# Kernel optimization log

Hardware: AMD Instinct MI355X
Metric: run time of the kernel (lower is better)

## Reference

```python
import jax, jax.numpy as jnp
import numpy as np

S, L, T, E, H = 88, 10, 30, 768, 64  # stocks, lookback days, texts/day, embed, hidden


def setup_inputs() -> dict:
    ks = iter(jax.random.split(jax.random.key(0), 40))

    def p(shape, s=0.05):
        return (jax.random.normal(next(ks), shape) * s).astype(jnp.float32)

    inp = {
        'text_inputs': jax.random.normal(next(ks), (S, L, T, E), jnp.float32),
        'time_inputs': jax.random.uniform(next(ks), (S, L, T), jnp.float32),
        # per-stock TimeLSTM params (torch Linear stored as [in,out])
        'Wd_w': p((S, H, H)), 'Wd_b': p((S, H)),
        'Wall_w': p((S, H, 4 * H)), 'Wall_b': p((S, 4 * H)),
        'Uall_w': p((S, E, 4 * H)), 'Uall_b': p((S, 4 * H)),
        # per-stock text attention
        'tW1_w': p((S, H, H)), 'tW1_b': p((S, H)),
        'tW2_w': p((S, H, H)), 'tW2_b': p((S, H)),
        'tV_w': p((S, H, 1)), 'tV_b': p((S, 1)),
        # per-stock day nn.LSTM cell (h0=0 so W_hh contributes nothing; keep its bias)
        'ih_w': p((S, H, 4 * H)), 'ih_b': p((S, 4 * H)), 'hh_b': p((S, 4 * H)),
        # per-stock day attention
        'dW1_w': p((S, H, H)), 'dW1_b': p((S, H)),
        'dW2_w': p((S, H, H)), 'dW2_b': p((S, H)),
        'dV_w': p((S, H, 1)), 'dV_b': p((S, 1)),
        # shared prediction head
        'pred_w': p((H, 1)), 'pred_b': p((1,)),
    }
    return inp


def _fast_forward(text_inputs, time_inputs, Wd_w, Wd_b, Wall_w, Wall_b, Uall_w, Uall_b,
                  tW1_w, tW1_b, tW2_w, tW2_b, tV_w, tV_b,
                  ih_w, ih_b, hh_b, dW1_w, dW1_b, dW2_w, dW2_b, dV_w, dV_b,
                  pred_w, pred_b):
    # Precompute input projection U_all(x): [S,L,T,4H]
    u = jnp.einsum('slte,seg->sltg', text_inputs, Uall_w) + Uall_b[:, None, None, :]

    def step(carry, xs):
        h, c = carry                      # each [S,L,H]
        u_t, ts_t = xs                    # [S,L,4H], [S,L]
        c_s1 = jnp.tanh(jnp.einsum('slh,shk->slk', c, Wd_w) + Wd_b[:, None, :])
        c_adj = c - c_s1 + c_s1 * ts_t[..., None]
        gates = jnp.einsum('slh,shg->slg', h, Wall_w) + Wall_b[:, None, :] + u_t
        f, i, o, g = jnp.split(jax.nn.sigmoid(gates), 4, axis=-1)  # all sigmoid (incl. candidate, as in source)
        c = f * c_adj + i * g
        h = o * jnp.tanh(c)
        return (h, c), h

    z = jnp.zeros((S, L, H), text_inputs.dtype)
    (h_last, _), hs = jax.lax.scan(step, (z, z), (jnp.moveaxis(u, 2, 0), jnp.moveaxis(time_inputs, 2, 0)))
    full = jnp.moveaxis(hs, 0, 2)  # [S,L,T,H]

    # text attention: softmax over texts T
    a1 = jnp.einsum('slh,shk->slk', h_last, tW1_w) + tW1_b[:, None, :]
    a2 = jnp.einsum('slth,shk->sltk', full, tW2_w) + tW2_b[:, None, None, :]
    score = jnp.einsum('slth,sho->slto', jnp.tanh(a1[:, :, None, :] + a2), tV_w) + tV_b[:, None, None, :]
    attn = jax.nn.softmax(score, axis=2)
    day_vec = jnp.sum(attn * full, axis=2)  # [S,L,H]

    # day nn.LSTM: input (1,L,64) seq-first => seq_len=1, batch=L -> single step from zero state
    gates = jnp.einsum('slh,shg->slg', day_vec, ih_w) + ih_b[:, None, :] + hh_b[:, None, :]
    i_g, f_g, g_g, o_g = jnp.split(gates, 4, axis=-1)  # torch gate order i,f,g,o
    c_d = jax.nn.sigmoid(i_g) * jnp.tanh(g_g)
    h_d = jax.nn.sigmoid(o_g) * jnp.tanh(c_d)  # [S,L,H]; output == h_n since seq_len==1

    # day attention: full == last == h_d, softmax over days L
    b1 = jnp.einsum('slh,shk->slk', h_d, dW1_w) + dW1_b[:, None, :]
    b2 = jnp.einsum('slh,shk->slk', h_d, dW2_w) + dW2_b[:, None, :]
    score_d = jnp.einsum('slh,sho->slo', jnp.tanh(b1 + b2), dV_w) + dV_b[:, None, :]
    attn_d = jax.nn.softmax(score_d, axis=1)
    stock_vec = jnp.sum(attn_d * h_d, axis=1)  # [S,H]

    return jax.nn.leaky_relu(stock_vec @ pred_w + pred_b)  # [S,1], slope 0.01


def reference(text_inputs, time_inputs, Wd_w, Wd_b, Wall_w, Wall_b, Uall_w, Uall_b,
              tW1_w, tW1_b, tW2_w, tW2_b, tV_w, tV_b,
              ih_w, ih_b, hh_b, dW1_w, dW1_b, dW2_w, dW2_b, dV_w, dV_b,
              pred_w, pred_b):
    return _fast_forward(text_inputs, time_inputs, Wd_w, Wd_b, Wall_w, Wall_b, Uall_w, Uall_b,
                         tW1_w, tW1_b, tW2_w, tW2_b, tV_w, tV_b,
                         ih_w, ih_b, hh_b, dW1_w, dW1_b, dW2_w, dW2_b, dV_w, dV_b,
                         pred_w, pred_b)
```

## Files before the change

kernel.cpp:

```cpp
#include <hip/hip_runtime.h>
#include <cmath>

#define NS 88
#define NL 10
#define NT 30
#define NE 768
#define NH 64
#define NG 256
#define NM 300

typedef _Float16 half_t;
typedef __attribute__((ext_vector_type(2))) _Float16 half2_t;
typedef __attribute__((ext_vector_type(8))) _Float16 half8;
typedef __attribute__((ext_vector_type(4))) _Float16 half4v;
typedef __attribute__((ext_vector_type(4))) float f32x4;

__device__ inline void gload_lds16(const void* g, void* l) {
  __builtin_amdgcn_global_load_lds(
      (const __attribute__((address_space(1))) unsigned int*)g,
      (__attribute__((address_space(3))) unsigned int*)l, 16, 0, 0);
}

__device__ inline float fsigmoid(float x) {
  return __builtin_amdgcn_rcpf(1.f + __expf(-x));
}
__device__ inline float ftanh(float x) {
  float e = __expf(2.f * x);
  return 1.f - 2.f * __builtin_amdgcn_rcpf(e + 1.f);
}

#if __has_builtin(__builtin_amdgcn_fdot2)
__device__ inline float fdot2(half2_t a, half2_t b, float c) {
  return __builtin_amdgcn_fdot2(a, b, c, false);
}
#else
__device__ inline float fdot2(half2_t a, half2_t b, float c) {
  return fmaf((float)a[1], (float)b[1], fmaf((float)a[0], (float)b[0], c));
}
#endif

__device__ inline half2_t mk_h2(float a, float b) {
  half2_t r; r[0] = (half_t)a; r[1] = (half_t)b; return r;
}

__global__ __launch_bounds__(256) void convB_kernel(
    const float* __restrict__ in, half_t* __restrict__ out)
{
  __shared__ float tile[32][36];
  int b  = blockIdx.x;
  int s  = b / 192;
  int r  = b % 192;
  int kt = r / 8;
  int nt = r % 8;
  int t  = threadIdx.x;

  int kk  = t >> 3;
  int nn4 = (t & 7) * 4;
  float4 v = *(const float4*)(in + ((size_t)s * NE + kt * 32 + kk) * NG + nt * 32 + nn4);
  tile[kk][nn4 + 0] = v.x; tile[kk][nn4 + 1] = v.y;
  tile[kk][nn4 + 2] = v.z; tile[kk][nn4 + 3] = v.w;
  __syncthreads();

  int nn = t >> 3;
  int kq = (t & 7) * 4;
  half4v o;
#pragma unroll
  for (int j = 0; j < 4; ++j) o[j] = (half_t)tile[kq + j][nn];
  *(half4v*)(out + ((size_t)s * NG + nt * 32 + nn) * NE + kt * 32 + kq) = o;
}

__global__ __launch_bounds__(256) void gemm_mfma_kernel(
    const float*  __restrict__ text,
    const half_t* __restrict__ Bf16,
    const float*  __restrict__ bias,
    float* __restrict__ U)
{
  __shared__ uint4 smem4[1536];
  char* smem = (char*)smem4;

  int b   = blockIdx.x;
  int swz = (b & 7) * 110 + (b >> 3);
  int s   = swz / 10;
  int rr_ = swz % 10;
  int m0  = (rr_ >> 1) * 64;
  int n0  = (rr_ & 1) * 128;

  int tid = threadIdx.x;
  int w = tid >> 6, l = tid & 63;
  int wm = w >> 1, wn = w & 1;
  int lr = l & 15, lk = l >> 4;

  const float*  At = text + (size_t)s * NM * NE;
  const half_t* Bb = Bf16 + ((size_t)s * NG + n0) * NE;

  f32x4 acc[2][4];
#pragma unroll
  for (int i = 0; i < 2; ++i)
#pragma unroll
    for (int j = 0; j < 4; ++j) acc[i][j] = (f32x4){0.f, 0.f, 0.f, 0.f};

  for (int step = 0; step < 12; ++step) {
    int k0 = step * 64;
#pragma unroll
    for (int j = 0; j < 4; ++j) {
      int ci  = j * 256 + tid;
      int row = ci >> 3;
      int c   = (ci & 7) ^ (row & 7);
      gload_lds16(Bb + (size_t)row * NE + k0 + c * 8,
                  smem + 8192 + j * 4096 + w * 1024);
    }
#pragma unroll
    for (int j = 0; j < 2; ++j) {
      int idx = j * 256 + tid;
      int row = idx >> 3, c = idx & 7;
      int m   = m0 + row;
      half8 av;
      if (m < NM) {
        const float* p = At + (size_t)m * NE + k0 + c * 8;
        float4 x = *(const float4*)p;
        float4 y = *(const float4*)(p + 4);
        av[0] = (half_t)x.x; av[1] = (half_t)x.y;
        av[2] = (half_t)x.z; av[3] = (half_t)x.w;
        av[4] = (half_t)y.x; av[5] = (half_t)y.y;
        av[6] = (half_t)y.z; av[7] = (half_t)y.w;
      } else {
#pragma unroll
        for (int q = 0; q < 8; ++q) av[q] = (half_t)0.f;
      }
      *(half8*)(smem + row * 128 + ((c ^ (row & 7)) * 16)) = av;
    }
    __syncthreads();

#pragma unroll
    for (int kk = 0; kk < 2; ++kk) {
      half8 af[2], bf[4];
#pragma unroll
      for (int fm = 0; fm < 2; ++fm) {
        int rw = wm * 32 + fm * 16 + lr;
        int cc = (kk * 4 + lk) ^ (rw & 7);
        af[fm] = *(const half8*)(smem + rw * 128 + cc * 16);
      }
#pragma unroll
      for (int fn = 0; fn < 4; ++fn) {
        int rw = wn * 64 + fn * 16 + lr;
        int cc = (kk * 4 + lk) ^ (rw & 7);
        bf[fn] = *(const half8*)(smem + 8192 + rw * 128 + cc * 16);
      }
#pragma unroll
      for (int fm = 0; fm < 2; ++fm)
#pragma unroll
        for (int fn = 0; fn < 4; ++fn)
          acc[fm][fn] = __builtin_amdgcn_mfma_f32_16x16x32_f16(
              af[fm], bf[fn], acc[fm][fn], 0, 0, 0);
    }
    __syncthreads();
  }

#pragma unroll
  for (int fn = 0; fn < 4; ++fn) {
    int col = n0 + wn * 64 + fn * 16 + lr;
    float bv = bias[(size_t)s * NG + col];
#pragma unroll
    for (int fm = 0; fm < 2; ++fm) {
      int mbase = m0 + wm * 32 + fm * 16 + lk * 4;
#pragma unroll
      for (int e = 0; e < 4; ++e) {
        int m = mbase + e;
        if (m < NM)
          U[((size_t)s * NM + m) * NG + col] = acc[fm][fn][e] + bv;
      }
    }
  }
}

__global__ __launch_bounds__(64) void lstm_attn_kernel(
    const float* __restrict__ u,
    const float* __restrict__ time_in,
    const float* __restrict__ Wdw,  const float* __restrict__ Wdb,
    const float* __restrict__ Wallw, const float* __restrict__ Wallb,
    const float* __restrict__ tW1w, const float* __restrict__ tW1b,
    const float* __restrict__ tW2w, const float* __restrict__ tW2b,
    const float* __restrict__ tVw,  const float* __restrict__ tVb,
    float* __restrict__ day_vec)
{
  int bid = blockIdx.x;
  int s = bid / NL;
  int j = threadIdx.x;

  __shared__ float   u_s[NT * NG];
  __shared__ float   hist[NT][NH];
  __shared__ float   ts_s[NT];
  __shared__ half2_t h2_s[NH / 2];
  __shared__ half2_t c2_s[NH / 2];

  const float* u_base = u + (size_t)bid * NT * NG;
#pragma unroll
  for (int i = 0; i < NT; ++i)
    gload_lds16(u_base + i * NG + j * 4, (char*)u_s + i * 1024);

  if (j < NT) ts_s[j] = time_in[(size_t)bid * NT + j];
  ((half_t*)h2_s)[j] = (half_t)0.f;
  ((half_t*)c2_s)[j] = (half_t)0.f;

  const float* Wa  = Wallw + (size_t)s * NH * NG;
  const float* Wdp = Wdw   + (size_t)s * NH * NH;
  half2_t wf[32], wi[32], wo[32], wg[32], wd[32];
#pragma unroll
  for (int k2 = 0; k2 < 32; ++k2) {
    wf[k2] = mk_h2(Wa[(2*k2) * NG + j],        Wa[(2*k2+1) * NG + j]);
    wi[k2] = mk_h2(Wa[(2*k2) * NG + 64 + j],   Wa[(2*k2+1) * NG + 64 + j]);
    wo[k2] = mk_h2(Wa[(2*k2) * NG + 128 + j],  Wa[(2*k2+1) * NG + 128 + j]);
    wg[k2] = mk_h2(Wa[(2*k2) * NG + 192 + j],  Wa[(2*k2+1) * NG + 192 + j]);
    wd[k2] = mk_h2(Wdp[(2*k2) * NH + j],       Wdp[(2*k2+1) * NH + j]);
  }
  float bf = Wallb[(size_t)s * NG + j];
  float bi = Wallb[(size_t)s * NG + 64 + j];
  float bo = Wallb[(size_t)s * NG + 128 + j];
  float bg = Wallb[(size_t)s * NG + 192 + j];
  float bd = Wdb[(size_t)s * NH + j];

  asm volatile("s_waitcnt vmcnt(0)" ::: "memory");

  float c_my = 0.f;
  for (int t = 0; t < NT; ++t) {
    float accf = bf + u_s[t * NG + j];
    float acci = bi + u_s[t * NG + 64 + j];
    float acco = bo + u_s[t * NG + 128 + j];
    float accg = bg + u_s[t * NG + 192 + j];
    float accd = bd;
#pragma unroll
    for (int k2 = 0; k2 < 32; ++k2) {
      half2_t hv = h2_s[k2];
      half2_t cv = c2_s[k2];
      accf = fdot2(hv, wf[k2], accf);
      acci = fdot2(hv, wi[k2], acci);
      acco = fdot2(hv, wo[k2], acco);
      accg = fdot2(hv, wg[k2], accg);
      accd = fdot2(cv, wd[k2], accd);
    }
    float f  = fsigmoid(accf);
    float ii = fsigmoid(acci);
    float o  = fsigmoid(acco);
    float gg = fsigmoid(accg);
    float cadj = c_my + ftanh(accd) * (ts_s[t] - 1.f);
    float cn = fmaf(f, cadj, ii * gg);
    c_my = cn;
    float hn = o * ftanh(cn);
    ((half_t*)h2_s)[j] = (half_t)hn;
    ((half_t*)c2_s)[j] = (half_t)cn;
    hist[t][j] = hn;
  }

  const float* tW1p = tW1w + (size_t)s * NH * NH;
  const float* tW2p = tW2w + (size_t)s * NH * NH;

  float tw2c[NH];
#pragma unroll
  for (int h = 0; h < NH; ++h) tw2c[h] = tW2p[(size_t)h * NH + j];

  float a1 = tW1b[(size_t)s * NH + j];
  {
    const float4* h4 = (const float4*)&hist[NT - 1][0];
#pragma unroll
    for (int q = 0; q < NH / 4; ++q) {
      float4 v = h4[q];
      a1 = fmaf(v.x, tW1p[(size_t)(4*q+0) * NH + j], a1);
      a1 = fmaf(v.y, tW1p[(size_t)(4*q+1) * NH + j], a1);
      a1 = fmaf(v.z, tW1p[(size_t)(4*q+2) * NH + j], a1);
      a1 = fmaf(v.w, tW1p[(size_t)(4*q+3) * NH + j], a1);
    }
  }
  float b2k = tW2b[(size_t)s * NH + j];
  float tv  = tVw[(size_t)s * NH + j];
  float tvb = tVb[s];

  float sc[NT];
#pragma unroll
  for (int t = 0; t < NT; ++t) {
    float a2 = b2k;
    const float4* h4 = (const float4*)&hist[t][0];
#pragma unroll
    for (int q = 0; q < NH / 4; ++q) {
      float4 v = h4[q];
      a2 = fmaf(v.x, tw2c[4*q+0], a2);
      a2 = fmaf(v.y, tw2c[4*q+1], a2);
      a2 = fmaf(v.z, tw2c[4*q+2], a2);
      a2 = fmaf(v.w, tw2c[4*q+3], a2);
    }
    float v = ftanh(a1 + a2) * tv;
#pragma unroll
    for (int off = 32; off >= 1; off >>= 1) v += __shfl_xor(v, off);
    sc[t] = v + tvb;
  }
  float mx = sc[0];
#pragma unroll
  for (int t = 1; t < NT; ++t) mx = fmaxf(mx, sc[t]);
  float sum = 0.f;
#pragma unroll
  for (int t = 0; t < NT; ++t) { sc[t] = __expf(sc[t] - mx); sum += sc[t]; }
  float inv = __builtin_amdgcn_rcpf(sum);
  float dv = 0.f;
#pragma unroll
  for (int t = 0; t < NT; ++t) dv = fmaf(sc[t] * inv, hist[t][j], dv);
  day_vec[(size_t)bid * NH + j] = dv;
}

__global__ __launch_bounds__(256) void day_head_kernel(
    const float* __restrict__ day_vec,
    const float* __restrict__ ihw, const float* __restrict__ ihb,
    const float* __restrict__ hhb,
    const float* __restrict__ dW1w, const float* __restrict__ dW1b,
    const float* __restrict__ dW2w, const float* __restrict__ dW2b,
    const float* __restrict__ dVw,  const float* __restrict__ dVb,
    const float* __restrict__ predw, const float* __restrict__ predb,
    float* __restrict__ out)
{
  int s = blockIdx.x;
  int g = threadIdx.x;
  int j = g & 63;
  int q = g >> 6;

  __shared__ float dv_s[NL][NH];
  __shared__ float gl[NL][NG];
  __shared__ float hd[NL][NH];

  for (int i = g; i < NL * NH; i += 256)
    ((float*)dv_s)[i] = day_vec[(size_t)s * NL * NH + i];
  __syncthreads();

  float ihcol[NH];
#pragma unroll
  for (int k = 0; k < NH; ++k)
    ihcol[k] = ihw[((size_t)s * NH + k) * NG + g];
  float bias = ihb[(size_t)s * NG + g] + hhb[(size_t)s * NG + g];

  bool is_gpart = (g >= 128 && g < 192);
  for (int l = 0; l < NL; ++l) {
    float acc = bias;
#pragma unroll
    for (int k = 0; k < NH; ++k) acc = fmaf(dv_s[l][k], ihcol[k], acc);
    gl[l][g] = is_gpart ? ftanh(acc) : fsigmoid(acc);
  }
  __syncthreads();
  for (int l = q; l < NL; l += 4) {
    float cd = gl[l][j] * gl[l][128 + j];
    hd[l][j] = gl[l][192 + j] * ftanh(cd);
  }
  __syncthreads();

  if (g < 64) {
    int k = g;
    float dw1c[NH], dw2c[NH];
#pragma unroll
    for (int h = 0; h < NH; ++h) {
      dw1c[h] = dW1w[((size_t)s * NH + h) * NH + k];
      dw2c[h] = dW2w[((size_t)s * NH + h) * NH + k];
    }
    float b1 = dW1b[(size_t)s * NH + k];
    float b2 = dW2b[(size_t)s * NH + k];
    float dv = dVw[(size_t)s * NH + k];
    float dvb = dVb[s];

    float sc[NL];
#pragma unroll
    for (int l = 0; l < NL; ++l) {
      float x1 = b1, x2 = b2;
#pragma unroll
      for (int h = 0; h < NH; ++h) {
        x1 = fmaf(hd[l][h], dw1c[h], x1);
        x2 = fmaf(hd[l][h], dw2c[h], x2);
      }
      float v = ftanh(x1 + x2) * dv;
#pragma unroll
      for (int off = 32; off >= 1; off >>= 1) v += __shfl_xor(v, off);
      sc[l] = v + dvb;
    }
    float mx = sc[0];
#pragma unroll
    for (int l = 1; l < NL; ++l) mx = fmaxf(mx, sc[l]);
    float sum = 0.f;
#pragma unroll
    for (int l = 0; l < NL; ++l) { sc[l] = __expf(sc[l] - mx); sum += sc[l]; }
    float inv = __builtin_amdgcn_rcpf(sum);
    float sv = 0.f;
#pragma unroll
    for (int l = 0; l < NL; ++l) sv = fmaf(sc[l] * inv, hd[l][k], sv);

    float p = sv * predw[k];
#pragma unroll
    for (int off = 32; off >= 1; off >>= 1) p += __shfl_xor(p, off);
    if (k == 0) {
      float x = p + predb[0];
      out[s] = (x >= 0.f) ? x : 0.01f * x;
    }
  }
}

extern "C" void kernel_launch(void* const* d_in, const int* in_sizes, int n_in,
                              void* d_out, int out_size, void* d_ws, size_t ws_size,
                              hipStream_t stream) {
  (void)in_sizes; (void)n_in; (void)out_size; (void)ws_size;

  const float* text    = (const float*)d_in[0];
  const float* time_in = (const float*)d_in[1];
  const float* Wdw     = (const float*)d_in[2];
  const float* Wdb     = (const float*)d_in[3];
  const float* Wallw   = (const float*)d_in[4];
  const float* Wallb   = (const float*)d_in[5];
  const float* Uallw   = (const float*)d_in[6];
  const float* Uallb   = (const float*)d_in[7];
  const float* tW1w    = (const float*)d_in[8];
  const float* tW1b    = (const float*)d_in[9];
  const float* tW2w    = (const float*)d_in[10];
  const float* tW2b    = (const float*)d_in[11];
  const float* tVw     = (const float*)d_in[12];
  const float* tVb     = (const float*)d_in[13];
  const float* ihw     = (const float*)d_in[14];
  const float* ihb     = (const float*)d_in[15];
  const float* hhb     = (const float*)d_in[16];
  const float* dW1w    = (const float*)d_in[17];
  const float* dW1b    = (const float*)d_in[18];
  const float* dW2w    = (const float*)d_in[19];
  const float* dW2b    = (const float*)d_in[20];
  const float* dVw     = (const float*)d_in[21];
  const float* dVb     = (const float*)d_in[22];
  const float* predw   = (const float*)d_in[23];
  const float* predb   = (const float*)d_in[24];

  float* ws      = (float*)d_ws;
  float* u       = ws;
  float* day_vec = u + (size_t)NS * NM * NG;
  half_t* Bf16   = (half_t*)(day_vec + (size_t)NS * NL * NH);

  convB_kernel<<<NS * 192, 256, 0, stream>>>(Uallw, Bf16);
  gemm_mfma_kernel<<<NS * 10, 256, 0, stream>>>(text, Bf16, Uallb, u);
  lstm_attn_kernel<<<NS * NL, 64, 0, stream>>>(u, time_in, Wdw, Wdb,
                                               Wallw, Wallb,
                                               tW1w, tW1b, tW2w, tW2b,
                                               tVw, tVb, day_vec);
  day_head_kernel<<<NS, 256, 0, stream>>>(day_vec, ihw, ihb, hhb,
                                          dW1w, dW1b, dW2w, dW2b, dVw, dVb,
                                          predw, predb, (float*)d_out);
}
```

Before: 104.7 us.

## Fuse U-projection GEMM into per-(stock,day) LSTM kernel, keeping U in LDS

Merges the MFMA GEMM producing the input projection into the TimeLSTM kernel. Each block computes the 30x256 projection for one (stock, day) directly into shared memory, then one wave runs the recurrence. This removes the global write and re-read of the large U tensor and one kernel launch. In exchange, each block reloads the full per-stock fp16 weight matrix, raising L2 traffic tenfold, pads 30 rows to 32, and idles three waves during the recurrence.

Result: slower. 136.3 us (+30.1%).

```diff
diff --git a/kernel.cpp b/kernel.cpp
--- a/kernel.cpp
+++ b/kernel.cpp
@@ -69,112 +69,10 @@
   *(half4v*)(out + ((size_t)s * NG + nt * 32 + nn) * NE + kt * 32 + kq) = o;
 }
 
-__global__ __launch_bounds__(256) void gemm_mfma_kernel(
+__global__ __launch_bounds__(256, 2) void fused_kernel(
     const float*  __restrict__ text,
     const half_t* __restrict__ Bf16,
-    const float*  __restrict__ bias,
-    float* __restrict__ U)
-{
-  __shared__ uint4 smem4[1536];
-  char* smem = (char*)smem4;
-
-  int b   = blockIdx.x;
-  int swz = (b & 7) * 110 + (b >> 3);
-  int s   = swz / 10;
-  int rr_ = swz % 10;
-  int m0  = (rr_ >> 1) * 64;
-  int n0  = (rr_ & 1) * 128;
-
-  int tid = threadIdx.x;
-  int w = tid >> 6, l = tid & 63;
-  int wm = w >> 1, wn = w & 1;
-  int lr = l & 15, lk = l >> 4;
-
-  const float*  At = text + (size_t)s * NM * NE;
-  const half_t* Bb = Bf16 + ((size_t)s * NG + n0) * NE;
-
-  f32x4 acc[2][4];
-#pragma unroll
-  for (int i = 0; i < 2; ++i)
-#pragma unroll
-    for (int j = 0; j < 4; ++j) acc[i][j] = (f32x4){0.f, 0.f, 0.f, 0.f};
-
-  for (int step = 0; step < 12; ++step) {
-    int k0 = step * 64;
-#pragma unroll
-    for (int j = 0; j < 4; ++j) {
-      int ci  = j * 256 + tid;
-      int row = ci >> 3;
-      int c   = (ci & 7) ^ (row & 7);
-      gload_lds16(Bb + (size_t)row * NE + k0 + c * 8,
-                  smem + 8192 + j * 4096 + w * 1024);
-    }
-#pragma unroll
-    for (int j = 0; j < 2; ++j) {
-      int idx = j * 256 + tid;
-      int row = idx >> 3, c = idx & 7;
-      int m   = m0 + row;
-      half8 av;
-      if (m < NM) {
-        const float* p = At + (size_t)m * NE + k0 + c * 8;
-        float4 x = *(const float4*)p;
-        float4 y = *(const float4*)(p + 4);
-        av[0] = (half_t)x.x; av[1] = (half_t)x.y;
-        av[2] = (half_t)x.z; av[3] = (half_t)x.w;
-        av[4] = (half_t)y.x; av[5] = (half_t)y.y;
-        av[6] = (half_t)y.z; av[7] = (half_t)y.w;
-      } else {
-#pragma unroll
-        for (int q = 0; q < 8; ++q) av[q] = (half_t)0.f;
-      }
-      *(half8*)(smem + row * 128 + ((c ^ (row & 7)) * 16)) = av;
-    }
-    __syncthreads();
-
-#pragma unroll
-    for (int kk = 0; kk < 2; ++kk) {
-      half8 af[2], bf[4];
-#pragma unroll
-      for (int fm = 0; fm < 2; ++fm) {
-        int rw = wm * 32 + fm * 16 + lr;
-        int cc = (kk * 4 + lk) ^ (rw & 7);
-        af[fm] = *(const half8*)(smem + rw * 128 + cc * 16);
-      }
-#pragma unroll
-      for (int fn = 0; fn < 4; ++fn) {
-        int rw = wn * 64 + fn * 16 + lr;
-        int cc = (kk * 4 + lk) ^ (rw & 7);
-        bf[fn] = *(const half8*)(smem + 8192 + rw * 128 + cc * 16);
-      }
-#pragma unroll
-      for (int fm = 0; fm < 2; ++fm)
-#pragma unroll
-        for (int fn = 0; fn < 4; ++fn)
-          acc[fm][fn] = __builtin_amdgcn_mfma_f32_16x16x32_f16(
-              af[fm], bf[fn], acc[fm][fn], 0, 0, 0);
-    }
-    __syncthreads();
-  }
-
-#pragma unroll
-  for (int fn = 0; fn < 4; ++fn) {
-    int col = n0 + wn * 64 + fn * 16 + lr;
-    float bv = bias[(size_t)s * NG + col];
-#pragma unroll
-    for (int fm = 0; fm < 2; ++fm) {
-      int mbase = m0 + wm * 32 + fm * 16 + lk * 4;
-#pragma unroll
-      for (int e = 0; e < 4; ++e) {
-        int m = mbase + e;
-        if (m < NM)
-          U[((size_t)s * NM + m) * NG + col] = acc[fm][fn][e] + bv;
-      }
-    }
-  }
-}
-
-__global__ __launch_bounds__(64) void lstm_attn_kernel(
-    const float* __restrict__ u,
+    const float*  __restrict__ ubias,
     const float* __restrict__ time_in,
     const float* __restrict__ Wdw,  const float* __restrict__ Wdb,
     const float* __restrict__ Wallw, const float* __restrict__ Wallb,
@@ -183,22 +81,108 @@
     const float* __restrict__ tVw,  const float* __restrict__ tVb,
     float* __restrict__ day_vec)
 {
-  int bid = blockIdx.x;
-  int s = bid / NL;
-  int j = threadIdx.x;
-
-  __shared__ float   u_s[NT * NG];
+  __shared__ float   u_s[32 * NG];
+  __shared__ uint4   Bbuf4[2048];
+  __shared__ uint4   Abuf4[256];
   __shared__ float   hist[NT][NH];
   __shared__ float   ts_s[NT];
   __shared__ half2_t h2_s[NH / 2];
   __shared__ half2_t c2_s[NH / 2];
-
-  const float* u_base = u + (size_t)bid * NT * NG;
-#pragma unroll
-  for (int i = 0; i < NT; ++i)
-    gload_lds16(u_base + i * NG + j * 4, (char*)u_s + i * 1024);
-
-  if (j < NT) ts_s[j] = time_in[(size_t)bid * NT + j];
+  char* Bbuf = (char*)Bbuf4;
+  char* Abuf = (char*)Abuf4;
+
+  int b   = blockIdx.x;
+  int bid = (b & 7) * 110 + (b >> 3);
+  int s   = bid / NL;
+  int tid = threadIdx.x;
+  int w = tid >> 6, l = tid & 63;
+  int lr = l & 15, lk = l >> 4;
+
+  const float*  At = text + (size_t)bid * NT * NE;
+  const half_t* Bb = Bf16 + (size_t)s * NG * NE;
+
+  if (tid < NT) ts_s[tid] = time_in[(size_t)bid * NT + tid];
+
+  f32x4 acc[2][4];
+#pragma unroll
+  for (int i = 0; i < 2; ++i)
+#pragma unroll
+    for (int j = 0; j < 4; ++j) acc[i][j] = (f32x4){0.f, 0.f, 0.f, 0.f};
+
+#pragma unroll 1
+  for (int step = 0; step < 12; ++step) {
+    int k0 = step * 64;
+#pragma unroll
+    for (int j = 0; j < 8; ++j) {
+      int ci  = j * 256 + tid;
+      int row = ci >> 3;
+      int c   = (ci & 7) ^ (row & 7);
+      gload_lds16(Bb + (size_t)row * NE + k0 + c * 8,
+                  Bbuf + j * 4096 + w * 1024);
+    }
+    {
+      int row = tid >> 3, c = tid & 7;
+      half8 av;
+      if (row < NT) {
+        const float* p = At + (size_t)row * NE + k0 + c * 8;
+        float4 x = *(const float4*)p;
+        float4 y = *(const float4*)(p + 4);
+        av[0] = (half_t)x.x; av[1] = (half_t)x.y;
+        av[2] = (half_t)x.z; av[3] = (half_t)x.w;
+        av[4] = (half_t)y.x; av[5] = (half_t)y.y;
+        av[6] = (half_t)y.z; av[7] = (half_t)y.w;
+      } else {
+#pragma unroll
+        for (int q = 0; q < 8; ++q) av[q] = (half_t)0.f;
+      }
+      *(half8*)(Abuf + row * 128 + ((c ^ (row & 7)) * 16)) = av;
+    }
+    __syncthreads();
+
+#pragma unroll
+    for (int kk = 0; kk < 2; ++kk) {
+      half8 af[2], bf[4];
+#pragma unroll
+      for (int fm = 0; fm < 2; ++fm) {
+        int rw = fm * 16 + lr;
+        int cc = (kk * 4 + lk) ^ (rw & 7);
+        af[fm] = *(const half8*)(Abuf + rw * 128 + cc * 16);
+      }
+#pragma unroll
+      for (int fn = 0; fn < 4; ++fn) {
+        int rw = w * 64 + fn * 16 + lr;
+        int cc = (kk * 4 + lk) ^ (rw & 7);
+        bf[fn] = *(const half8*)(Bbuf + rw * 128 + cc * 16);
+      }
+#pragma unroll
+      for (int fm = 0; fm < 2; ++fm)
+#pragma unroll
+        for (int fn = 0; fn < 4; ++fn)
+          acc[fm][fn] = __builtin_amdgcn_mfma_f32_16x16x32_f16(
+              af[fm], bf[fn], acc[fm][fn], 0, 0, 0);
+    }
+    __syncthreads();
+  }
+
+#pragma unroll
+  for (int fn = 0; fn < 4; ++fn) {
+    int col = w * 64 + fn * 16 + lr;
+    float bv = ubias[(size_t)s * NG + col];
+#pragma unroll
+    for (int fm = 0; fm < 2; ++fm) {
+      int rbase = fm * 16 + lk * 4;
+#pragma unroll
+      for (int e = 0; e < 4; ++e) {
+        int row = rbase + e;
+        if (row < NT) u_s[row * NG + col] = acc[fm][fn][e] + bv;
+      }
+    }
+  }
+  __syncthreads();
+
+  if (w != 0) return;
+  int j = l;
+
   ((half_t*)h2_s)[j] = (half_t)0.f;
   ((half_t*)c2_s)[j] = (half_t)0.f;
 
@@ -213,21 +197,19 @@
     wg[k2] = mk_h2(Wa[(2*k2) * NG + 192 + j],  Wa[(2*k2+1) * NG + 192 + j]);
     wd[k2] = mk_h2(Wdp[(2*k2) * NH + j],       Wdp[(2*k2+1) * NH + j]);
   }
-  float bf = Wallb[(size_t)s * NG + j];
-  float bi = Wallb[(size_t)s * NG + 64 + j];
-  float bo = Wallb[(size_t)s * NG + 128 + j];
-  float bg = Wallb[(size_t)s * NG + 192 + j];
-  float bd = Wdb[(size_t)s * NH + j];
-
-  asm volatile("s_waitcnt vmcnt(0)" ::: "memory");
+  float bf_ = Wallb[(size_t)s * NG + j];
+  float bi_ = Wallb[(size_t)s * NG + 64 + j];
+  float bo_ = Wallb[(size_t)s * NG + 128 + j];
+  float bg_ = Wallb[(size_t)s * NG + 192 + j];
+  float bd_ = Wdb[(size_t)s * NH + j];
 
   float c_my = 0.f;
   for (int t = 0; t < NT; ++t) {
-    float accf = bf + u_s[t * NG + j];
-    float acci = bi + u_s[t * NG + 64 + j];
-    float acco = bo + u_s[t * NG + 128 + j];
-    float accg = bg + u_s[t * NG + 192 + j];
-    float accd = bd;
+    float accf = bf_ + u_s[t * NG + j];
+    float acci = bi_ + u_s[t * NG + 64 + j];
+    float acco = bo_ + u_s[t * NG + 128 + j];
+    float accg = bg_ + u_s[t * NG + 192 + j];
+    float accd = bd_;
 #pragma unroll
     for (int k2 = 0; k2 < 32; ++k2) {
       half2_t hv = h2_s[k2];
@@ -428,16 +410,14 @@
   const float* predb   = (const float*)d_in[24];
 
   float* ws      = (float*)d_ws;
-  float* u       = ws;
-  float* day_vec = u + (size_t)NS * NM * NG;
+  float* day_vec = ws;
   half_t* Bf16   = (half_t*)(day_vec + (size_t)NS * NL * NH);
 
   convB_kernel<<<NS * 192, 256, 0, stream>>>(Uallw, Bf16);
-  gemm_mfma_kernel<<<NS * 10, 256, 0, stream>>>(text, Bf16, Uallb, u);
-  lstm_attn_kernel<<<NS * NL, 64, 0, stream>>>(u, time_in, Wdw, Wdb,
-                                               Wallw, Wallb,
-                                               tW1w, tW1b, tW2w, tW2b,
-                                               tVw, tVb, day_vec);
+  fused_kernel<<<NS * NL, 256, 0, stream>>>(text, Bf16, Uallb, time_in,
+                                            Wdw, Wdb, Wallw, Wallb,
+                                            tW1w, tW1b, tW2w, tW2b,
+                                            tVw, tVb, day_vec);
   day_head_kernel<<<NS, 256, 0, stream>>>(day_vec, ihw, ihb, hhb,
                                           dW1w, dW1b, dW2w, dW2b, dVw, dVb,
                                           predw, predb, (float*)d_out);
```

## Retile U-projection GEMM per (stock,day) with full-K A tile in LDS

Applied to the files above, without the earlier changes.

The GEMM is retiled so each block handles one (stock, day) pair: 30 rows padded to 32 and all 256 gate columns, with each wave owning 64 columns. The whole fp16 A tile over full K is staged once in swizzled LDS, which removes the per-K-step barriers. B fragments are now read straight from global/L2 instead of being staged through LDS. Occupancy is hinted at 3 blocks/CU. The risks are uncoalesced direct B loads and padded rows wasting MFMA work, since 32 rows are computed for 30 used.

New measurement: 135.5 us. +29.4%, slower.

```diff
diff --git a/kernel.cpp b/kernel.cpp
--- a/kernel.cpp
+++ b/kernel.cpp
@@ -69,28 +69,45 @@
   *(half4v*)(out + ((size_t)s * NG + nt * 32 + nn) * NE + kt * 32 + kq) = o;
 }
 
-__global__ __launch_bounds__(256) void gemm_mfma_kernel(
+__global__ __launch_bounds__(256, 3) void gemm_mfma_kernel(
     const float*  __restrict__ text,
     const half_t* __restrict__ Bf16,
-    const float*  __restrict__ bias,
+    const float*  __restrict__ ubias,
     float* __restrict__ U)
 {
-  __shared__ uint4 smem4[1536];
-  char* smem = (char*)smem4;
+  __shared__ char Albuf[32 * 1536];
 
   int b   = blockIdx.x;
-  int swz = (b & 7) * 110 + (b >> 3);
-  int s   = swz / 10;
-  int rr_ = swz % 10;
-  int m0  = (rr_ >> 1) * 64;
-  int n0  = (rr_ & 1) * 128;
-
+  int bid = (b & 7) * 110 + (b >> 3);
+  int s   = bid / NL;
   int tid = threadIdx.x;
   int w = tid >> 6, l = tid & 63;
-  int wm = w >> 1, wn = w & 1;
   int lr = l & 15, lk = l >> 4;
 
-  const float*  At = text + (size_t)s * NM * NE;
+  const float* At = text + (size_t)bid * NT * NE;
+
+#pragma unroll
+  for (int i = 0; i < 24; ++i) {
+    int idx = i * 256 + tid;
+    int e   = idx * 4;
+    int row = e / NE;
+    int col = e % NE;
+    half4v hv;
+    if (row < NT) {
+      float4 v = *(const float4*)(At + (size_t)row * NE + col);
+      hv[0] = (half_t)v.x; hv[1] = (half_t)v.y;
+      hv[2] = (half_t)v.z; hv[3] = (half_t)v.w;
+    } else {
+      hv[0] = (half_t)0.f; hv[1] = (half_t)0.f;
+      hv[2] = (half_t)0.f; hv[3] = (half_t)0.f;
+    }
+    int chunk = col >> 3;
+    int swz   = (chunk & ~7) | ((chunk & 7) ^ (row & 7));
+    *(half4v*)(Albuf + (size_t)row * 1536 + swz * 16 + ((col & 7) ? 8 : 0)) = hv;
+  }
+  __syncthreads();
+
+  int n0 = w * 64;
   const half_t* Bb = Bf16 + ((size_t)s * NG + n0) * NE;
 
   f32x4 acc[2][4];
@@ -99,75 +116,41 @@
 #pragma unroll
     for (int j = 0; j < 4; ++j) acc[i][j] = (f32x4){0.f, 0.f, 0.f, 0.f};
 
-  for (int step = 0; step < 12; ++step) {
-    int k0 = step * 64;
-#pragma unroll
-    for (int j = 0; j < 4; ++j) {
-      int ci  = j * 256 + tid;
-      int row = ci >> 3;
-      int c   = (ci & 7) ^ (row & 7);
-      gload_lds16(Bb + (size_t)row * NE + k0 + c * 8,
-                  smem + 8192 + j * 4096 + w * 1024);
-    }
-#pragma unroll
-    for (int j = 0; j < 2; ++j) {
-      int idx = j * 256 + tid;
-      int row = idx >> 3, c = idx & 7;
-      int m   = m0 + row;
-      half8 av;
-      if (m < NM) {
-        const float* p = At + (size_t)m * NE + k0 + c * 8;
-        float4 x = *(const float4*)p;
-        float4 y = *(const float4*)(p + 4);
-        av[0] = (half_t)x.x; av[1] = (half_t)x.y;
-        av[2] = (half_t)x.z; av[3] = (half_t)x.w;
-        av[4] = (half_t)y.x; av[5] = (half_t)y.y;
-        av[6] = (half_t)y.z; av[7] = (half_t)y.w;
-      } else {
-#pragma unroll
-        for (int q = 0; q < 8; ++q) av[q] = (half_t)0.f;
-      }
-      *(half8*)(smem + row * 128 + ((c ^ (row & 7)) * 16)) = av;
-    }
-    __syncthreads();
-
-#pragma unroll
-    for (int kk = 0; kk < 2; ++kk) {
-      half8 af[2], bf[4];
-#pragma unroll
-      for (int fm = 0; fm < 2; ++fm) {
-        int rw = wm * 32 + fm * 16 + lr;
-        int cc = (kk * 4 + lk) ^ (rw & 7);
-        af[fm] = *(const half8*)(smem + rw * 128 + cc * 16);
-      }
-#pragma unroll
-      for (int fn = 0; fn < 4; ++fn) {
-        int rw = wn * 64 + fn * 16 + lr;
-        int cc = (kk * 4 + lk) ^ (rw & 7);
-        bf[fn] = *(const half8*)(smem + 8192 + rw * 128 + cc * 16);
-      }
-#pragma unroll
-      for (int fm = 0; fm < 2; ++fm)
-#pragma unroll
-        for (int fn = 0; fn < 4; ++fn)
-          acc[fm][fn] = __builtin_amdgcn_mfma_f32_16x16x32_f16(
-              af[fm], bf[fn], acc[fm][fn], 0, 0, 0);
-    }
-    __syncthreads();
-  }
-
+#pragma unroll 4
+  for (int ks = 0; ks < 24; ++ks) {
+    half8 af[2], bf[4];
+#pragma unroll
+    for (int fm = 0; fm < 2; ++fm) {
+      int row   = fm * 16 + lr;
+      int chunk = ks * 4 + lk;
+      int swz   = (chunk & ~7) | ((chunk & 7) ^ (row & 7));
+      af[fm] = *(const half8*)(Albuf + (size_t)row * 1536 + swz * 16);
+    }
+#pragma unroll
+    for (int fn = 0; fn < 4; ++fn) {
+      bf[fn] = *(const half8*)(Bb + (size_t)(fn * 16 + lr) * NE +
+                               ks * 32 + lk * 8);
+    }
+#pragma unroll
+    for (int fm = 0; fm < 2; ++fm)
+#pragma unroll
+      for (int fn = 0; fn < 4; ++fn)
+        acc[fm][fn] = __builtin_amdgcn_mfma_f32_16x16x32_f16(
+            af[fm], bf[fn], acc[fm][fn], 0, 0, 0);
+  }
+
+  float* Ub = U + (size_t)bid * NT * NG;
 #pragma unroll
   for (int fn = 0; fn < 4; ++fn) {
-    int col = n0 + wn * 64 + fn * 16 + lr;
-    float bv = bias[(size_t)s * NG + col];
+    int col = n0 + fn * 16 + lr;
+    float bv = ubias[(size_t)s * NG + col];
 #pragma unroll
     for (int fm = 0; fm < 2; ++fm) {
-      int mbase = m0 + wm * 32 + fm * 16 + lk * 4;
+      int rbase = fm * 16 + lk * 4;
 #pragma unroll
       for (int e = 0; e < 4; ++e) {
-        int m = mbase + e;
-        if (m < NM)
-          U[((size_t)s * NM + m) * NG + col] = acc[fm][fn][e] + bv;
+        int row = rbase + e;
+        if (row < NT) Ub[(size_t)row * NG + col] = acc[fm][fn][e] + bv;
       }
     }
   }
@@ -433,7 +416,7 @@
   half_t* Bf16   = (half_t*)(day_vec + (size_t)NS * NL * NH);
 
   convB_kernel<<<NS * 192, 256, 0, stream>>>(Uallw, Bf16);
-  gemm_mfma_kernel<<<NS * 10, 256, 0, stream>>>(text, Bf16, Uallb, u);
+  gemm_mfma_kernel<<<NS * NL, 256, 0, stream>>>(text, Bf16, Uallb, u);
   lstm_attn_kernel<<<NS * NL, 64, 0, stream>>>(u, time_in, Wdw, Wdb,
                                                Wallw, Wallb,
                                                tW1w, tW1b, tW2w, tW2b,
```
